# Performance work log

Hardware: AMD Instinct MI355X
Metric: run time of the kernel (lower is better)

Reference implementation:

```python
import jax, jax.numpy as jnp
import numpy as np

KERNEL_NUM = 20

def _l2norm(x):
    # torch F.normalize: x / max(||x||, eps)
    n = jnp.sqrt(jnp.sum(x * x, axis=-1, keepdims=True))
    return x / jnp.maximum(n, 1e-12)

def setup_inputs() -> dict:
    key = jax.random.key(0)
    ks = jax.random.split(key, 5)
    B, C, H, S, E, V = 32, 5, 50, 20, 300, 60000
    return {
        "candidate_title": jax.random.randint(ks[0], (B, C, S), 0, V),
        "clicked_title": jax.random.randint(ks[1], (B, H, S), 0, V),
        "candidate_title_pad": jnp.ones((B, C, S), jnp.float32),
        "clicked_title_pad": jnp.ones((B, H, S), jnp.float32),
        "embedding": jax.random.normal(ks[2], (V, E), jnp.float32),
        "ltr_w": jax.random.normal(ks[3], (H * KERNEL_NUM, 1), jnp.float32) * 0.03,
        "ltr_b": jax.random.normal(ks[4], (1,), jnp.float32),
    }

def reference(candidate_title, clicked_title, candidate_title_pad, clicked_title_pad, embedding, ltr_w, ltr_b):
    B, C, S = candidate_title.shape
    H = clicked_title.shape[1]
    K = KERNEL_NUM
    dt = embedding.dtype
    mus = (-0.9 + 0.1 * jnp.arange(K, dtype=dt))                    # [K]
    sigmas = jnp.concatenate([jnp.full((K - 1,), 0.1, dt), jnp.full((1,), 0.001, dt)])
    cdd = _l2norm(embedding[candidate_title])                        # [B,C,S,E]
    his = _l2norm(embedding[clicked_title])                          # [B,H,S,E]
    sim = jnp.einsum('bcse,bhte->bchst', cdd, his)                   # [B,C,H,S,S]
    mask_his = clicked_title_pad[:, None, :, None, :, None]          # [B,1,H,1,S,1]
    mask_cdd = candidate_title_pad[:, :, None, :, None]              # [B,C,1,S,1]
    kern = jnp.exp(-((sim[..., None] - mus) ** 2) / (2.0 * sigmas ** 2)) * mask_his  # [B,C,H,S,S,K]
    pooling_sum = jnp.sum(kern, axis=4)                              # [B,C,H,S,K]
    log_pooling = jnp.log(jnp.clip(pooling_sum, 1e-10, None)) * mask_cdd * 0.01
    pooling_vectors = jnp.sum(log_pooling, axis=-2)                  # [B,C,H,K]
    score = pooling_vectors.reshape(B, C, H * K) @ ltr_w + ltr_b     # [B,C,1]
    score = jax.nn.log_softmax(score, axis=1)                        # cdd_size > 1 path
    return jnp.squeeze(score)                                        # [B,C]
```

## Files before the change

### kernel.cpp

```cpp
#include <hip/hip_runtime.h>
#include <hip/hip_fp16.h>

typedef _Float16 half8 __attribute__((ext_vector_type(8)));
typedef _Float16 half4v __attribute__((ext_vector_type(4)));
typedef float float4v __attribute__((ext_vector_type(4)));

#define E_DIM 300
#define KP 320
#define B_ 32
#define NROW_CDD 3200
#define NROW_HIS 32000

__global__ __launch_bounds__(256) void gather_norm(const int* __restrict__ cand,
                                                   const int* __restrict__ clk,
                                                   const float* __restrict__ emb,
                                                   _Float16* __restrict__ outH)
{
    int row  = blockIdx.x * 4 + (threadIdx.x >> 6);
    int lane = threadIdx.x & 63;
    int tok = (row < NROW_CDD) ? cand[row] : clk[row - NROW_CDD];
    const float* e = emb + (long)tok * E_DIM;
    float v[5];
    float ss = 0.f;
#pragma unroll
    for (int j = 0; j < 5; ++j) {
        int idx = lane + j * 64;
        float x = (idx < E_DIM) ? e[idx] : 0.f;
        v[j] = x;
        ss += x * x;
    }
#pragma unroll
    for (int off = 32; off; off >>= 1) ss += __shfl_xor(ss, off);
    float scale = 1.0f / fmaxf(sqrtf(ss), 1e-12f);
    _Float16* o = outH + (long)row * KP;
#pragma unroll
    for (int j = 0; j < 5; ++j) {
        int idx = lane + j * 64;
        o[idx] = (_Float16)((idx < E_DIM) ? v[j] * scale : 0.f);
    }
}

__global__ __launch_bounds__(448, 2) void sim_gemm(const _Float16* __restrict__ wsH,
                                                   _Float16* __restrict__ simW)
{
    __shared__ __align__(16) char Bbuf[64 * 640 + 128];
    __shared__ _Float16 simT[100 * 66];

    int b = blockIdx.y, ntile = blockIdx.x;
    int tid = threadIdx.x;
    int wave = tid >> 6, lane = tid & 63;
    int g4 = lane >> 4, r16 = lane & 15;

    const char* gA = (const char*)(wsH + (size_t)b * 100 * KP);
    const char* gB = (const char*)(wsH + (size_t)(NROW_CDD + b * 1000) * KP);

    int rA = wave * 16 + r16; if (rA > 99) rA = 99;
    const char* pA = gA + (size_t)rA * 640;
    half8 af[10];
#pragma unroll
    for (int k = 0; k < 10; ++k) af[k] = *(const half8*)(pA + k * 64 + g4 * 16);

    uint4 bv[6];
#pragma unroll
    for (int j = 0; j < 6; ++j) {
        int u = tid + 448 * j; if (u > 2559) u = 2559;
        int r = u / 40;
        int gr = ntile * 64 + r; if (gr > 999) gr = 999;
        bv[j] = *(const uint4*)(gB + (size_t)(gr * 40 + (u - r * 40)) * 16);
    }
#pragma unroll
    for (int j = 0; j < 6; ++j) {
        int u = tid + 448 * j;
        if (u < 2560) {
            int r = u / 40;
            *(uint4*)(Bbuf + ((u * 16) ^ ((r & 7) << 4))) = bv[j];
        }
    }
    __syncthreads();

    float4v acc[4];
#pragma unroll
    for (int n = 0; n < 4; ++n) acc[n] = (float4v){0.f, 0.f, 0.f, 0.f};

#pragma unroll
    for (int k = 0; k < 10; ++k) {
#pragma unroll
        for (int n = 0; n < 4; ++n) {
            int rB = n * 16 + r16;
            half8 bf = *(const half8*)(Bbuf + ((rB * 640 + k * 64 + g4 * 16) ^ ((rB & 7) << 4)));
            acc[n] = __builtin_amdgcn_mfma_f32_16x16x32_f16(af[k], bf, acc[n], 0, 0, 0);
        }
    }

#pragma unroll
    for (int n = 0; n < 4; ++n) {
#pragma unroll
        for (int j = 0; j < 4; ++j) {
            int r = wave * 16 + g4 * 4 + j;
            if (r < 100) simT[r * 66 + n * 16 + r16] = (_Float16)acc[n][j];
        }
    }
    __syncthreads();

    size_t obase = (size_t)b * 100000 + (size_t)ntile * 64;
    for (int u = tid; u < 6400; u += 448) {
        int r = u >> 6, c = u & 63;
        int gcol = ntile * 64 + c;
        if (gcol < 1000) simW[(size_t)(b * 100 + r) * 1000 + ntile * 64 + c] = simT[r * 66 + c];
    }
    (void)obase;
}

__global__ __launch_bounds__(256) void knrm_pool(const _Float16* __restrict__ simW,
                                                 const float* __restrict__ cpad,
                                                 const float* __restrict__ hpad,
                                                 const float* __restrict__ ltr_w,
                                                 float* __restrict__ rowsum)
{
    __shared__ float sS[50 * 21];
    __shared__ float mS[50 * 21];
    __shared__ float wS[1000];
    __shared__ float part[4];

    int row = blockIdx.x;
    int b = row / 100;
    int tid = threadIdx.x;

    if (tid < 250) {
        int p = tid * 4;
        half4v hv = *(const half4v*)(simW + (size_t)row * 1000 + p);
        float4v mv = *(const float4v*)(hpad + (size_t)b * 1000 + p);
        *(float4v*)&wS[p] = *(const float4v*)(ltr_w + p);
#pragma unroll
        for (int q = 0; q < 4; ++q) {
            int pq = p + q, h = pq / 20, t = pq - h * 20;
            sS[h * 21 + t] = (float)hv[q];
            mS[h * 21 + t] = mv[q];
        }
    }
    __syncthreads();

    float val = 0.f;
    if (tid < 250) {
        int h = tid % 50, kq = tid / 50;
        float bj[4], cj[4];
        bool is19[4];
#pragma unroll
        for (int j = 0; j < 4; ++j) {
            float mu = -0.9f + 0.1f * (float)(kq * 4 + j);
            bj[j] = 100.0f * mu;
            cj[j] = -50.0f * mu * mu;
            is19[j] = (kq * 4 + j) == 19;
        }
        float psum0 = 0.f, psum1 = 0.f, psum2 = 0.f, psum3 = 0.f;
        const float* sp = sS + h * 21;
        const float* mp = mS + h * 21;
#pragma unroll 4
        for (int t = 0; t < 20; ++t) {
            float s  = sp[t];
            float mm = mp[t];
            float d  = s - 1.0f;
            float arg19 = -500000.0f * d * d;
            float a0 = is19[0] ? arg19 : fmaf(fmaf(-50.0f, s, bj[0]), s, cj[0]);
            float a1 = is19[1] ? arg19 : fmaf(fmaf(-50.0f, s, bj[1]), s, cj[1]);
            float a2 = is19[2] ? arg19 : fmaf(fmaf(-50.0f, s, bj[2]), s, cj[2]);
            float a3 = is19[3] ? arg19 : fmaf(fmaf(-50.0f, s, bj[3]), s, cj[3]);
            psum0 = fmaf(__expf(a0), mm, psum0);
            psum1 = fmaf(__expf(a1), mm, psum1);
            psum2 = fmaf(__expf(a2), mm, psum2);
            psum3 = fmaf(__expf(a3), mm, psum3);
        }
        const float* wp = wS + h * 20 + kq * 4;
        val  = __logf(fmaxf(psum0, 1e-10f)) * wp[0];
        val += __logf(fmaxf(psum1, 1e-10f)) * wp[1];
        val += __logf(fmaxf(psum2, 1e-10f)) * wp[2];
        val += __logf(fmaxf(psum3, 1e-10f)) * wp[3];
    }
#pragma unroll
    for (int off = 32; off; off >>= 1) val += __shfl_down(val, off);
    int wave = tid >> 6, lane = tid & 63;
    if (lane == 0) part[wave] = val;
    __syncthreads();
    if (tid == 0)
        rowsum[row] = (part[0] + part[1] + part[2] + part[3]) * 0.01f * cpad[row];
}

__global__ __launch_bounds__(64) void finalize(const float* __restrict__ rowsum,
                                               const float* __restrict__ ltr_b,
                                               float* __restrict__ out)
{
    int b = blockIdx.x;
    int tid = threadIdx.x;
    __shared__ float sc[5];
    if (tid < 5) {
        float a = ltr_b[0];
        const float* rp = rowsum + (b * 5 + tid) * 20;
#pragma unroll
        for (int s = 0; s < 20; ++s) a += rp[s];
        sc[tid] = a;
    }
    __syncthreads();
    if (tid < 5) {
        float m = fmaxf(fmaxf(fmaxf(sc[0], sc[1]), fmaxf(sc[2], sc[3])), sc[4]);
        float sum = 0.f;
#pragma unroll
        for (int i = 0; i < 5; ++i) sum += __expf(sc[i] - m);
        out[b * 5 + tid] = sc[tid] - m - __logf(sum);
    }
}

extern "C" void kernel_launch(void* const* d_in, const int* in_sizes, int n_in,
                              void* d_out, int out_size, void* d_ws, size_t ws_size,
                              hipStream_t stream)
{
    const int*   cand = (const int*)d_in[0];
    const int*   clk  = (const int*)d_in[1];
    const float* cpad = (const float*)d_in[2];
    const float* hpad = (const float*)d_in[3];
    const float* emb  = (const float*)d_in[4];
    const float* lw   = (const float*)d_in[5];
    const float* lb   = (const float*)d_in[6];
    float* out = (float*)d_out;

    _Float16* wsH  = (_Float16*)d_ws;
    _Float16* simW = (_Float16*)((char*)d_ws + (size_t)(NROW_CDD + NROW_HIS) * KP * 2);
    float* rowsum  = (float*)((char*)simW + (size_t)B_ * 100 * 1000 * 2);

    hipLaunchKernelGGL(gather_norm, dim3((NROW_CDD + NROW_HIS) / 4), dim3(256), 0, stream,
                       cand, clk, emb, wsH);
    hipLaunchKernelGGL(sim_gemm, dim3(16, B_), dim3(448), 0, stream, wsH, simW);
    hipLaunchKernelGGL(knrm_pool, dim3(NROW_CDD), dim3(256), 0, stream,
                       simW, cpad, hpad, lw, rowsum);
    hipLaunchKernelGGL(finalize, dim3(B_), dim3(64), 0, stream, rowsum, lb, out);
}
```

Baseline: 45.19 us.

## Fuse history embedding gather and normalization into the similarity GEMM

The clicked-title embeddings are no longer gathered, normalized and written as fp16 to a 32000-row workspace by a separate pass. Each sim_gemm block now loads its 64 history rows straight from the embedding table, converts the raw values to fp16 into LDS, and computes each row's inverse norm. That scale is applied to the accumulator after the MFMA. This removes a large workspace write and re-read. In exchange, the fp16 operands are unnormalized, which slightly changes rounding, and the GEMM kernel now carries gather latency.

```diff
diff --git a/kernel.cpp b/kernel.cpp
--- a/kernel.cpp
+++ b/kernel.cpp
@@ -9,17 +9,15 @@
 #define KP 320
 #define B_ 32
 #define NROW_CDD 3200
-#define NROW_HIS 32000
 
 __global__ __launch_bounds__(256) void gather_norm(const int* __restrict__ cand,
-                                                   const int* __restrict__ clk,
                                                    const float* __restrict__ emb,
                                                    _Float16* __restrict__ outH)
 {
     int row  = blockIdx.x * 4 + (threadIdx.x >> 6);
     int lane = threadIdx.x & 63;
-    int tok = (row < NROW_CDD) ? cand[row] : clk[row - NROW_CDD];
-    const float* e = emb + (long)tok * E_DIM;
+    int tok = cand[row];
+    const float* e = emb + (size_t)tok * E_DIM;
     float v[5];
     float ss = 0.f;
 #pragma unroll
@@ -32,7 +30,7 @@
 #pragma unroll
     for (int off = 32; off; off >>= 1) ss += __shfl_xor(ss, off);
     float scale = 1.0f / fmaxf(sqrtf(ss), 1e-12f);
-    _Float16* o = outH + (long)row * KP;
+    _Float16* o = outH + (size_t)row * KP;
 #pragma unroll
     for (int j = 0; j < 5; ++j) {
         int idx = lane + j * 64;
@@ -40,40 +38,52 @@
     }
 }
 
-__global__ __launch_bounds__(448, 2) void sim_gemm(const _Float16* __restrict__ wsH,
+__global__ __launch_bounds__(448, 2) void sim_gemm(const _Float16* __restrict__ wsA,
+                                                   const int* __restrict__ clk,
+                                                   const float* __restrict__ emb,
                                                    _Float16* __restrict__ simW)
 {
     __shared__ __align__(16) char Bbuf[64 * 640 + 128];
     __shared__ _Float16 simT[100 * 66];
+    __shared__ float invB[64];
 
     int b = blockIdx.y, ntile = blockIdx.x;
     int tid = threadIdx.x;
     int wave = tid >> 6, lane = tid & 63;
     int g4 = lane >> 4, r16 = lane & 15;
 
-    const char* gA = (const char*)(wsH + (size_t)b * 100 * KP);
-    const char* gB = (const char*)(wsH + (size_t)(NROW_CDD + b * 1000) * KP);
-
     int rA = wave * 16 + r16; if (rA > 99) rA = 99;
-    const char* pA = gA + (size_t)rA * 640;
+    const char* pA = (const char*)(wsA + (size_t)(b * 100 + rA) * KP);
     half8 af[10];
 #pragma unroll
     for (int k = 0; k < 10; ++k) af[k] = *(const half8*)(pA + k * 64 + g4 * 16);
 
-    uint4 bv[6];
-#pragma unroll
-    for (int j = 0; j < 6; ++j) {
-        int u = tid + 448 * j; if (u > 2559) u = 2559;
-        int r = u / 40;
-        int gr = ntile * 64 + r; if (gr > 999) gr = 999;
-        bv[j] = *(const uint4*)(gB + (size_t)(gr * 40 + (u - r * 40)) * 16);
-    }
-#pragma unroll
-    for (int j = 0; j < 6; ++j) {
-        int u = tid + 448 * j;
-        if (u < 2560) {
-            int r = u / 40;
-            *(uint4*)(Bbuf + ((u * 16) ^ ((r & 7) << 4))) = bv[j];
+#pragma unroll 2
+    for (int i = 0; i < 10; ++i) {
+        int r = wave * 10 + i;
+        if (r < 64) {
+            int col = ntile * 64 + r; if (col > 999) col = 999;
+            int tok = clk[b * 1000 + col];
+            const float4* e = (const float4*)(emb + (size_t)tok * E_DIM);
+            float4 v0 = e[lane];
+            float4 v1 = {0.f, 0.f, 0.f, 0.f};
+            if (lane < 11) v1 = e[64 + lane];
+            float ss = v0.x*v0.x + v0.y*v0.y + v0.z*v0.z + v0.w*v0.w
+                     + v1.x*v1.x + v1.y*v1.y + v1.z*v1.z + v1.w*v1.w;
+#pragma unroll
+            for (int o = 32; o; o >>= 1) ss += __shfl_xor(ss, o);
+            if (lane == 0) invB[r] = 1.0f / fmaxf(sqrtf(ss), 1e-12f);
+            int swz = (r & 7) << 4;
+            half4v h0 = { (_Float16)v0.x, (_Float16)v0.y, (_Float16)v0.z, (_Float16)v0.w };
+            *(half4v*)(Bbuf + ((r * 640 + lane * 8) ^ swz)) = h0;
+            if (lane < 11) {
+                half4v h1 = { (_Float16)v1.x, (_Float16)v1.y, (_Float16)v1.z, (_Float16)v1.w };
+                *(half4v*)(Bbuf + ((r * 640 + 512 + lane * 8) ^ swz)) = h1;
+            }
+            if (lane < 5) {
+                half4v hz = { (_Float16)0.f, (_Float16)0.f, (_Float16)0.f, (_Float16)0.f };
+                *(half4v*)(Bbuf + ((r * 640 + 600 + lane * 8) ^ swz)) = hz;
+            }
         }
     }
     __syncthreads();
@@ -94,21 +104,21 @@
 
 #pragma unroll
     for (int n = 0; n < 4; ++n) {
+        int lcol = n * 16 + r16;
+        float sc = invB[lcol];
 #pragma unroll
         for (int j = 0; j < 4; ++j) {
             int r = wave * 16 + g4 * 4 + j;
-            if (r < 100) simT[r * 66 + n * 16 + r16] = (_Float16)acc[n][j];
-        }
-    }
-    __syncthreads();
-
-    size_t obase = (size_t)b * 100000 + (size_t)ntile * 64;
+            if (r < 100) simT[r * 66 + lcol] = (_Float16)(acc[n][j] * sc);
+        }
+    }
+    __syncthreads();
+
     for (int u = tid; u < 6400; u += 448) {
         int r = u >> 6, c = u & 63;
         int gcol = ntile * 64 + c;
-        if (gcol < 1000) simW[(size_t)(b * 100 + r) * 1000 + ntile * 64 + c] = simT[r * 66 + c];
-    }
-    (void)obase;
+        if (gcol < 1000) simW[(size_t)(b * 100 + r) * 1000 + gcol] = simT[r * 66 + c];
+    }
 }
 
 __global__ __launch_bounds__(256) void knrm_pool(const _Float16* __restrict__ simW,
@@ -222,13 +232,14 @@
     const float* lb   = (const float*)d_in[6];
     float* out = (float*)d_out;
 
-    _Float16* wsH  = (_Float16*)d_ws;
-    _Float16* simW = (_Float16*)((char*)d_ws + (size_t)(NROW_CDD + NROW_HIS) * KP * 2);
+    _Float16* wsA  = (_Float16*)d_ws;
+    _Float16* simW = (_Float16*)((char*)d_ws + (size_t)NROW_CDD * KP * 2);
     float* rowsum  = (float*)((char*)simW + (size_t)B_ * 100 * 1000 * 2);
 
-    hipLaunchKernelGGL(gather_norm, dim3((NROW_CDD + NROW_HIS) / 4), dim3(256), 0, stream,
-                       cand, clk, emb, wsH);
-    hipLaunchKernelGGL(sim_gemm, dim3(16, B_), dim3(448), 0, stream, wsH, simW);
+    hipLaunchKernelGGL(gather_norm, dim3(NROW_CDD / 4), dim3(256), 0, stream,
+                       cand, emb, wsA);
+    hipLaunchKernelGGL(sim_gemm, dim3(16, B_), dim3(448), 0, stream,
+                       wsA, clk, emb, simW);
     hipLaunchKernelGGL(knrm_pool, dim3(NROW_CDD), dim3(256), 0, stream,
                        simW, cpad, hpad, lw, rowsum);
     hipLaunchKernelGGL(finalize, dim3(B_), dim3(64), 0, stream, rowsum, lb, out);
```

Measured after the change: 46.69 us. 3.3% more time.

## Vectorize gather loads and restructure sim GEMM into 4-wave two-half pipeline

Applied to the files above, without the earlier changes.

gather_norm now reads each embedding row with float4 loads and writes half4 vectors. This is valid because 300 floats per row keeps every row 16-byte aligned. sim_gemm drops from 7 to 4 waves, with each wave covering two M tiles so every B fragment load feeds two MFMAs. It splits the 64-column tile into two 32-column halves, prefetching the second half into registers while the first computes, and stores output as half4 instead of scalar halves. The aim is better LDS reuse, some load/compute overlap and wider global stores. The cost is fewer waves per block and redundant work for the duplicated M tile (wave 3, mi 1 clamps to tile 6).

```diff
diff --git a/kernel.cpp b/kernel.cpp
--- a/kernel.cpp
+++ b/kernel.cpp
@@ -19,34 +19,36 @@
     int row  = blockIdx.x * 4 + (threadIdx.x >> 6);
     int lane = threadIdx.x & 63;
     int tok = (row < NROW_CDD) ? cand[row] : clk[row - NROW_CDD];
-    const float* e = emb + (long)tok * E_DIM;
-    float v[5];
-    float ss = 0.f;
-#pragma unroll
-    for (int j = 0; j < 5; ++j) {
-        int idx = lane + j * 64;
-        float x = (idx < E_DIM) ? e[idx] : 0.f;
-        v[j] = x;
-        ss += x * x;
-    }
+    const float4* e4 = (const float4*)(emb + (size_t)tok * E_DIM);
+
+    float4 v0 = e4[lane];
+    float4 v1 = {0.f, 0.f, 0.f, 0.f};
+    if (lane < 11) v1 = e4[64 + lane];
+    float ss = v0.x*v0.x + v0.y*v0.y + v0.z*v0.z + v0.w*v0.w
+             + v1.x*v1.x + v1.y*v1.y + v1.z*v1.z + v1.w*v1.w;
 #pragma unroll
     for (int off = 32; off; off >>= 1) ss += __shfl_xor(ss, off);
-    float scale = 1.0f / fmaxf(sqrtf(ss), 1e-12f);
-    _Float16* o = outH + (long)row * KP;
-#pragma unroll
-    for (int j = 0; j < 5; ++j) {
-        int idx = lane + j * 64;
-        o[idx] = (_Float16)((idx < E_DIM) ? v[j] * scale : 0.f);
-    }
-}
-
-__global__ __launch_bounds__(448, 2) void sim_gemm(const _Float16* __restrict__ wsH,
+    float sc = 1.0f / fmaxf(sqrtf(ss), 1e-12f);
+
+    _Float16* o = outH + (size_t)row * KP;
+    half4v h0 = { (_Float16)(v0.x*sc), (_Float16)(v0.y*sc), (_Float16)(v0.z*sc), (_Float16)(v0.w*sc) };
+    *(half4v*)(o + 4 * lane) = h0;
+    if (lane < 11) {
+        half4v h1 = { (_Float16)(v1.x*sc), (_Float16)(v1.y*sc), (_Float16)(v1.z*sc), (_Float16)(v1.w*sc) };
+        *(half4v*)(o + 256 + 4 * lane) = h1;
+    } else if (lane < 16) {
+        half4v hz = { (_Float16)0.f, (_Float16)0.f, (_Float16)0.f, (_Float16)0.f };
+        *(half4v*)(o + 256 + 4 * lane) = hz;
+    }
+}
+
+__global__ __launch_bounds__(256, 2) void sim_gemm(const _Float16* __restrict__ wsH,
                                                    _Float16* __restrict__ simW)
 {
-    __shared__ __align__(16) char Bbuf[64 * 640 + 128];
-    __shared__ _Float16 simT[100 * 66];
-
-    int b = blockIdx.y, ntile = blockIdx.x;
+    __shared__ __align__(16) char Bbuf[2][32 * 640];
+    __shared__ _Float16 simT[100 * 36];
+
+    int b = blockIdx.y, ip = blockIdx.x;
     int tid = threadIdx.x;
     int wave = tid >> 6, lane = tid & 63;
     int g4 = lane >> 4, r16 = lane & 15;
@@ -54,61 +56,96 @@
     const char* gA = (const char*)(wsH + (size_t)b * 100 * KP);
     const char* gB = (const char*)(wsH + (size_t)(NROW_CDD + b * 1000) * KP);
 
-    int rA = wave * 16 + r16; if (rA > 99) rA = 99;
-    const char* pA = gA + (size_t)rA * 640;
-    half8 af[10];
-#pragma unroll
-    for (int k = 0; k < 10; ++k) af[k] = *(const half8*)(pA + k * 64 + g4 * 16);
-
-    uint4 bv[6];
-#pragma unroll
-    for (int j = 0; j < 6; ++j) {
-        int u = tid + 448 * j; if (u > 2559) u = 2559;
+    half8 af[2][10];
+#pragma unroll
+    for (int mi = 0; mi < 2; ++mi) {
+        int m = wave + 4 * mi; if (m > 6) m = 6;
+        int rA = m * 16 + r16; if (rA > 99) rA = 99;
+        const char* pA = gA + (size_t)rA * 640;
+#pragma unroll
+        for (int k = 0; k < 10; ++k) af[mi][k] = *(const half8*)(pA + k * 64 + g4 * 16);
+    }
+
+    uint4 bv[5];
+#pragma unroll
+    for (int j = 0; j < 5; ++j) {
+        int u = tid + 256 * j;
         int r = u / 40;
-        int gr = ntile * 64 + r; if (gr > 999) gr = 999;
-        bv[j] = *(const uint4*)(gB + (size_t)(gr * 40 + (u - r * 40)) * 16);
-    }
-#pragma unroll
-    for (int j = 0; j < 6; ++j) {
-        int u = tid + 448 * j;
-        if (u < 2560) {
-            int r = u / 40;
-            *(uint4*)(Bbuf + ((u * 16) ^ ((r & 7) << 4))) = bv[j];
-        }
-    }
-    __syncthreads();
-
-    float4v acc[4];
-#pragma unroll
-    for (int n = 0; n < 4; ++n) acc[n] = (float4v){0.f, 0.f, 0.f, 0.f};
-
-#pragma unroll
-    for (int k = 0; k < 10; ++k) {
-#pragma unroll
-        for (int n = 0; n < 4; ++n) {
-            int rB = n * 16 + r16;
-            half8 bf = *(const half8*)(Bbuf + ((rB * 640 + k * 64 + g4 * 16) ^ ((rB & 7) << 4)));
-            acc[n] = __builtin_amdgcn_mfma_f32_16x16x32_f16(af[k], bf, acc[n], 0, 0, 0);
-        }
-    }
-
-#pragma unroll
-    for (int n = 0; n < 4; ++n) {
-#pragma unroll
-        for (int j = 0; j < 4; ++j) {
-            int r = wave * 16 + g4 * 4 + j;
-            if (r < 100) simT[r * 66 + n * 16 + r16] = (_Float16)acc[n][j];
-        }
-    }
-    __syncthreads();
-
-    size_t obase = (size_t)b * 100000 + (size_t)ntile * 64;
-    for (int u = tid; u < 6400; u += 448) {
-        int r = u >> 6, c = u & 63;
-        int gcol = ntile * 64 + c;
-        if (gcol < 1000) simW[(size_t)(b * 100 + r) * 1000 + ntile * 64 + c] = simT[r * 66 + c];
-    }
-    (void)obase;
+        int col = ip * 64 + r; if (col > 999) col = 999;
+        bv[j] = *(const uint4*)(gB + (size_t)(col * 40 + (u - r * 40)) * 16);
+    }
+#pragma unroll
+    for (int j = 0; j < 5; ++j) {
+        int u = tid + 256 * j;
+        int r = u / 40;
+        *(uint4*)(&Bbuf[0][0] + ((u * 16) ^ ((r & 7) << 4))) = bv[j];
+    }
+#pragma unroll
+    for (int j = 0; j < 5; ++j) {
+        int u = tid + 256 * j;
+        int r = u / 40;
+        int col = ip * 64 + 32 + r; if (col > 999) col = 999;
+        bv[j] = *(const uint4*)(gB + (size_t)(col * 40 + (u - r * 40)) * 16);
+    }
+    __syncthreads();
+
+#pragma unroll
+    for (int half = 0; half < 2; ++half) {
+        float4v acc[2][2];
+#pragma unroll
+        for (int mi = 0; mi < 2; ++mi)
+#pragma unroll
+            for (int n = 0; n < 2; ++n) acc[mi][n] = (float4v){0.f, 0.f, 0.f, 0.f};
+
+#pragma unroll
+        for (int k = 0; k < 10; ++k) {
+#pragma unroll
+            for (int n = 0; n < 2; ++n) {
+                int rB = n * 16 + r16;
+                half8 bf = *(const half8*)(&Bbuf[half][0] +
+                               ((rB * 640 + k * 64 + g4 * 16) ^ ((rB & 7) << 4)));
+#pragma unroll
+                for (int mi = 0; mi < 2; ++mi)
+                    acc[mi][n] = __builtin_amdgcn_mfma_f32_16x16x32_f16(af[mi][k], bf, acc[mi][n], 0, 0, 0);
+            }
+        }
+
+#pragma unroll
+        for (int mi = 0; mi < 2; ++mi) {
+            int m = wave + 4 * mi; if (m > 6) m = 6;
+#pragma unroll
+            for (int n = 0; n < 2; ++n) {
+#pragma unroll
+                for (int j = 0; j < 4; ++j) {
+                    int r = m * 16 + g4 * 4 + j;
+                    if (r < 100) simT[r * 36 + n * 16 + r16] = (_Float16)acc[mi][n][j];
+                }
+            }
+        }
+        __syncthreads();
+
+        int cbase = ip * 64 + half * 32;
+#pragma unroll
+        for (int it = 0; it < 4; ++it) {
+            int u = tid + 256 * it;
+            if (u < 800) {
+                int r = u >> 3, c4 = u & 7;
+                int col = cbase + c4 * 4;
+                if (col < 1000)
+                    *(half4v*)(simW + (size_t)(b * 100 + r) * 1000 + col) =
+                        *(half4v*)(simT + r * 36 + c4 * 4);
+            }
+        }
+        if (half == 0) {
+#pragma unroll
+            for (int j = 0; j < 5; ++j) {
+                int u = tid + 256 * j;
+                int r = u / 40;
+                *(uint4*)(&Bbuf[1][0] + ((u * 16) ^ ((r & 7) << 4))) = bv[j];
+            }
+        }
+        __syncthreads();
+    }
 }
 
 __global__ __launch_bounds__(256) void knrm_pool(const _Float16* __restrict__ simW,
@@ -228,7 +265,7 @@
 
     hipLaunchKernelGGL(gather_norm, dim3((NROW_CDD + NROW_HIS) / 4), dim3(256), 0, stream,
                        cand, clk, emb, wsH);
-    hipLaunchKernelGGL(sim_gemm, dim3(16, B_), dim3(448), 0, stream, wsH, simW);
+    hipLaunchKernelGGL(sim_gemm, dim3(16, B_), dim3(256), 0, stream, wsH, simW);
     hipLaunchKernelGGL(knrm_pool, dim3(NROW_CDD), dim3(256), 0, stream,
                        simW, cpad, hpad, lw, rowsum);
     hipLaunchKernelGGL(finalize, dim3(B_), dim3(64), 0, stream, rowsum, lb, out);
```

Measured after the change: 49.28 us. 1.09x slower.
